# Performance work log

Hardware: AMD Instinct MI355X
Metric: run time of the kernel (lower is better)

## Reference

```python
import jax, jax.numpy as jnp
from jax import lax
import numpy as np

# cfg constants (not present in snippet; fixed realistic values)
GAMMA = 5.0            # cfg.RISK_AVERSION
COST_COEFF = 1e-3      # cfg.COST_COEFF
ALPHA = 0.95           # cfg.CVAR_CONFIDENCE
KAPPA = 2.0627128075074256  # norm.pdf(norm.ppf(0.95)) / (1 - 0.95)
PEN_XI = 100.0
N_ITERS = 500
LR = 0.01

B, H, N = 128, 12, 100


def setup_inputs() -> dict:
    key = jax.random.key(0)
    k1, k2, k3, k4 = jax.random.split(key, 4)
    mu = 0.02 * jax.random.normal(k1, (B, H, N), dtype=jnp.float32)
    # factor scale so that sigma_p = ||L^T w|| is O(0.02) for diversified w
    L = 0.02 * jax.random.normal(k2, (B, H, N, N), dtype=jnp.float32)
    w_prev = jax.random.uniform(k3, (B, N), dtype=jnp.float32)
    w_prev = w_prev / jnp.sum(w_prev, axis=-1, keepdims=True)  # on simplex
    cvar_limit = 0.05 + 0.05 * jax.random.uniform(k4, (B,), dtype=jnp.float32)
    return {"mu": mu, "L": L, "w_prev": w_prev, "cvar_limit": cvar_limit}


def _project_simplex(v):
    # Euclidean projection of each last-axis vector onto {w >= 0, sum w = 1}
    n = v.shape[-1]
    u = jnp.sort(v, axis=-1)[..., ::-1]
    cssv = jnp.cumsum(u, axis=-1) - 1.0
    ar = jnp.arange(1, n + 1, dtype=v.dtype)
    rho = jnp.sum(u * ar > cssv, axis=-1)          # >= 1 always
    theta = jnp.take_along_axis(cssv, (rho - 1)[..., None], axis=-1)
    theta = theta / rho[..., None].astype(v.dtype)
    return jnp.maximum(v - theta, 0.0)


def _neg_objective(w, mu, L, w_prev, cvar_limit):
    # w: (B,H,N). Exact-penalty reformulation: optimal xi_t = relu(-mu_p + kappa*sigma_p - limit)
    Lw = jnp.einsum('bhnm,bhn->bhm', L, w)             # L[t].T @ w[t]
    ret_t = jnp.einsum('bhn,bhn->bh', mu, w)           # mu[t] @ w[t]
    risk = jnp.sum(Lw * Lw, axis=(1, 2))               # sum_t ||L_t^T w_t||^2
    w_lag = jnp.concatenate([w_prev[:, None, :], w[:, :-1]], axis=1)
    diff = w - w_lag
    cost = jnp.sum(jnp.sqrt(diff * diff + 1e-10), axis=(1, 2))  # smoothed L1 turnover
    sigma = jnp.sqrt(jnp.sum(Lw * Lw, axis=-1) + 1e-12)          # (B,H)
    viol = jnp.maximum(-ret_t + KAPPA * sigma - cvar_limit[:, None], 0.0)
    obj = jnp.sum(ret_t, 1) - GAMMA * risk - COST_COEFF * cost - PEN_XI * jnp.sum(viol, 1)
    return -jnp.sum(obj)


def _solve(mu, L, w_prev, cvar_limit):
    b, h, n = mu.shape
    w0 = jnp.broadcast_to(w_prev[:, None, :], (b, h, n))
    grad_fn = jax.grad(_neg_objective)

    def step(w, _):
        g = grad_fn(w, mu, L, w_prev, cvar_limit)
        return _project_simplex(w - LR * g), None

    w, _ = lax.scan(jax.checkpoint(step), w0, None, length=N_ITERS)
    return w


def reference(mu, L, w_prev, cvar_limit):
    # Batched projected-gradient solver for the same convex MPO program the
    # original solves with SCS via CvxpyLayer; returns the optimal plan w (B,H,N).
    return _solve(mu, L, w_prev, cvar_limit)
```

## Files before the change

### kernel.cpp

```cpp
#include <hip/hip_runtime.h>
#include <cstdint>
#include <cstddef>

#define NIT    500
#define GAMMA_ 5.0f
#define CC_    1e-3f
#define KAPPA_ 2.0627128075074256f
#define PEN_   100.0f
#define LR_    0.01f

#define PBUF_BYTES (128*2*2*100*4)
#define FLAG_COUNT 256

#define VMFENCE() asm volatile("s_waitcnt vmcnt(0)" ::: "memory")
__device__ __forceinline__ float sysLoadF(float* p) {
  return __hip_atomic_fetch_add(p, 0.0f, __ATOMIC_RELAXED, __HIP_MEMORY_SCOPE_SYSTEM);
}
__device__ __forceinline__ void sysStoreF(float* p, float v) {
  (void)__hip_atomic_exchange(p, v, __ATOMIC_RELAXED, __HIP_MEMORY_SCOPE_SYSTEM);
}
__device__ __forceinline__ int sysLoadI(int* p) {
  return __hip_atomic_fetch_add(p, 0, __ATOMIC_RELAXED, __HIP_MEMORY_SCOPE_SYSTEM);
}
__device__ __forceinline__ void sysStoreI(int* p, int v) {
  (void)__hip_atomic_exchange(p, v, __ATOMIC_RELAXED, __HIP_MEMORY_SCOPE_SYSTEM);
}

__device__ __forceinline__ float rdlane(float v, int lane) {
  return __int_as_float(__builtin_amdgcn_readlane(__float_as_int(v), lane));
}

__device__ __forceinline__ float wred64(float x) {
  int t;
  t = __builtin_amdgcn_update_dpp(0, __float_as_int(x), 0x111, 0xf, 0xf, true); x += __int_as_float(t);
  t = __builtin_amdgcn_update_dpp(0, __float_as_int(x), 0x112, 0xf, 0xf, true); x += __int_as_float(t);
  t = __builtin_amdgcn_update_dpp(0, __float_as_int(x), 0x114, 0xf, 0xf, true); x += __int_as_float(t);
  t = __builtin_amdgcn_update_dpp(0, __float_as_int(x), 0x118, 0xf, 0xf, true); x += __int_as_float(t);
  t = __builtin_amdgcn_update_dpp(0, __float_as_int(x), 0x142, 0xa, 0xf, true); x += __int_as_float(t);
  t = __builtin_amdgcn_update_dpp(0, __float_as_int(x), 0x143, 0xc, 0xf, true); x += __int_as_float(t);
  return rdlane(x, 63);
}

__global__ __launch_bounds__(768, 1) void mpo_solver(
    const float* __restrict__ mu, const float* __restrict__ L,
    const float* __restrict__ wprev, const float* __restrict__ climit,
    float* __restrict__ out, float* __restrict__ pbuf, int* __restrict__ flags)
{
  const int tid  = threadIdx.x;
  const int lane = tid & 63;
  const int wave = __builtin_amdgcn_readfirstlane(tid >> 6);
  const int j    = wave >> 1;
  const int sec  = wave & 1;
  const int bid  = blockIdx.x;
  const int b    = bid & 127;
  const int half = bid >> 7;
  const int h    = half * 6 + j;
  const int bh   = b * 12 + h;

  __shared__ float wbuf[2][6][100];
  __shared__ float ybuf[6][100];

  const float* Lb = L + (size_t)bh * 10000;

  float S[100];
#pragma unroll
  for (int c = 0; c < 100; ++c) S[c] = 0.f;
  const int r = sec * 50 + lane;
  if (lane < 50) {
#pragma unroll 1
    for (int mc = 0; mc < 25; ++mc) {
      float4 lr = *(const float4*)(Lb + r * 100 + mc * 4);
#pragma unroll
      for (int c = 0; c < 100; ++c) {
        const float* Lc = Lb + c * 100 + mc * 4;
        S[c] = fmaf(lr.x, Lc[0], fmaf(lr.y, Lc[1], fmaf(lr.z, Lc[2], fmaf(lr.w, Lc[3], S[c]))));
      }
    }
  }

  const bool val1 = (lane < 36);
  float mu0 = mu[(size_t)bh * 100 + lane];
  float mu1 = val1 ? mu[(size_t)bh * 100 + 64 + lane] : 0.f;
  float wp0 = wprev[b * 100 + lane];
  float wp1 = val1 ? wprev[b * 100 + 64 + lane] : 0.f;
  float lim = climit[b];

  float w0 = wp0, w1 = wp1;

  if (sec == 0) {
    wbuf[0][j][lane] = wp0;
    if (val1) wbuf[0][j][64 + lane] = wp1;
  }
  __syncthreads();

  const bool hasNext = (h < 11);
  const bool isPubL  = (half == 0) && (j == 5);
  const bool isPubH  = (half == 1) && (j == 0);
  const int  flagPub = isPubL ? (b * 2 + 0) : (b * 2 + 1);
  const int  flagCon = isPubL ? (b * 2 + 1) : (b * 2 + 0);
  const bool isCon   = (sec == 0) && (isPubL || isPubH);
  bool dead = false;
  float thp = -3.0e38f;

  for (int k = 0; k < NIT; ++k) {
    const int p = k & 1;

    float yloc;
    {
      float a0 = 0.f, a1 = 0.f, a2 = 0.f, a3 = 0.f;
      const float* wrow = wbuf[p][j];
#pragma unroll
      for (int q = 0; q < 25; ++q) {
        float4 wq = *(const float4*)(wrow + q * 4);
        a0 = fmaf(wq.x, S[q * 4 + 0], a0);
        a1 = fmaf(wq.y, S[q * 4 + 1], a1);
        a2 = fmaf(wq.z, S[q * 4 + 2], a2);
        a3 = fmaf(wq.w, S[q * 4 + 3], a3);
      }
      yloc = (a0 + a2) + (a1 + a3);
      if (sec == 1 && lane < 50) ybuf[j][50 + lane] = yloc;
    }

    float pf0 = 0.f, pf1 = 0.f;
    bool pfReady = false;
    if (isCon && k > 0) {
      if (sysLoadI(&flags[flagCon]) >= k) {
        float* src = pbuf + ((size_t)flagCon * 2 + (k & 1)) * 100;
        pf0 = sysLoadF(&src[lane]);
        pf1 = val1 ? sysLoadF(&src[64 + lane]) : 0.f;
        pfReady = true;
      }
    }
    __syncthreads();

    if (sec == 0) {
      float y0 = (lane < 50) ? yloc : ybuf[j][lane];
      float y1 = val1 ? ybuf[j][64 + lane] : 0.f;

      float ret = wred64(fmaf(mu0, w0, mu1 * w1));
      float s2  = wred64(fmaf(y0, w0, y1 * w1));
      float sigma = sqrtf(s2 + 1e-12f);
      float z     = KAPPA_ * sigma - ret - lim;
      float act   = (z > 0.f) ? 1.f : 0.f;
      float cY    = 2.f * GAMMA_ + act * (PEN_ * KAPPA_ / sigma);
      float cM    = -(1.f + act * PEN_);

      float wl0, wl1, wn0 = 0.f, wn1 = 0.f;
      if (j == 0) {
        if (half == 0 || k == 0) { wl0 = wp0; wl1 = wp1; }
        else {
          if (!pfReady) {
            if (!dead) {
              long guard = 0;
              while (sysLoadI(&flags[flagCon]) < k) {
                __builtin_amdgcn_s_sleep(2);
                if (++guard > (1L << 17)) { dead = true; break; }
              }
            }
            float* src = pbuf + ((size_t)flagCon * 2 + (k & 1)) * 100;
            pf0 = sysLoadF(&src[lane]);
            pf1 = val1 ? sysLoadF(&src[64 + lane]) : 0.f;
          }
          wl0 = pf0; wl1 = pf1;
        }
      } else { wl0 = wbuf[p][j - 1][lane]; wl1 = val1 ? wbuf[p][j - 1][64 + lane] : 0.f; }
      if (hasNext) {
        if (j == 5) {
          if (k == 0) { wn0 = wp0; wn1 = wp1; }
          else {
            if (!pfReady) {
              if (!dead) {
                long guard = 0;
                while (sysLoadI(&flags[flagCon]) < k) {
                  __builtin_amdgcn_s_sleep(2);
                  if (++guard > (1L << 17)) { dead = true; break; }
                }
              }
              float* src = pbuf + ((size_t)flagCon * 2 + (k & 1)) * 100;
              pf0 = sysLoadF(&src[lane]);
              pf1 = val1 ? sysLoadF(&src[64 + lane]) : 0.f;
            }
            wn0 = pf0; wn1 = pf1;
          }
        } else { wn0 = wbuf[p][j + 1][lane]; wn1 = val1 ? wbuf[p][j + 1][64 + lane] : 0.f; }
      }

      float dw0 = w0 - wl0;
      float g0  = fmaf(cM, mu0, cY * y0) + CC_ * (dw0 * rsqrtf(fmaf(dw0, dw0, 1e-10f)));
      if (hasNext) { float dn0 = wn0 - w0; g0 -= CC_ * (dn0 * rsqrtf(fmaf(dn0, dn0, 1e-10f))); }
      float v0 = fmaf(-LR_, g0, w0);
      float v1 = 0.f;
      if (val1) {
        float dw1 = w1 - wl1;
        float g1  = fmaf(cM, mu1, cY * y1) + CC_ * (dw1 * rsqrtf(fmaf(dw1, dw1, 1e-10f)));
        if (hasNext) { float dn1 = wn1 - w1; g1 -= CC_ * (dn1 * rsqrtf(fmaf(dn1, dn1, 1e-10f))); }
        v1 = fmaf(-LR_, g1, w1);
      }

      float a1m = val1 ? 1.f : 0.f;
      float na0 = (v0 > thp) ? 1.f : 0.f;
      float na1 = (val1 && (v1 > thp)) ? 1.f : 0.f;
      float Ssum = wred64(na0 * v0 + na1 * v1);
      float Cnt  = wred64(na0 + na1);
      if (Cnt < 0.5f) { Ssum = wred64(v0 + a1m * v1); Cnt = 100.f; }
      float theta = (Ssum - 1.f) / Cnt;
      for (int it = 0; it < 112; ++it) {
        na0 = (v0 > theta) ? 1.f : 0.f;
        na1 = (val1 && (v1 > theta)) ? 1.f : 0.f;
        float ns = wred64(na0 * v0 + na1 * v1);
        float nc = wred64(na0 + na1);
        if (nc == Cnt && ns == Ssum) break;
        if (it == 7) {
          ns = wred64(v0 + a1m * v1);
          nc = 100.f;
        }
        Ssum = ns; Cnt = nc;
        theta = (Ssum - 1.f) / Cnt;
      }
      thp = theta;
      w0 = fmaxf(v0 - theta, 0.f);
      w1 = val1 ? fmaxf(v1 - theta, 0.f) : 0.f;

      wbuf[1 - p][j][lane] = w0;
      if (val1) wbuf[1 - p][j][64 + lane] = w1;

      if (isPubL || isPubH) {
        float* dst = pbuf + ((size_t)flagPub * 2 + ((k + 1) & 1)) * 100;
        sysStoreF(&dst[lane], w0);
        if (val1) sysStoreF(&dst[64 + lane], w1);
        if (lane == 0) {
          VMFENCE();
          sysStoreI(&flags[flagPub], k + 1);
        }
      }
    }
    __syncthreads();
  }

  if (sec == 0) {
    float* o = out + (size_t)bh * 100;
    o[lane] = w0;
    if (val1) o[64 + lane] = w1;
  }
}

extern "C" void kernel_launch(void* const* d_in, const int* in_sizes, int n_in,
                              void* d_out, int out_size, void* d_ws, size_t ws_size,
                              hipStream_t stream) {
  const float* mu = (const float*)d_in[0];
  const float* L  = (const float*)d_in[1];
  const float* wp = (const float*)d_in[2];
  const float* cl = (const float*)d_in[3];
  float* pbuf  = (float*)d_ws;
  int*   flags = (int*)((char*)d_ws + PBUF_BYTES);
  hipMemsetAsync(flags, 0, FLAG_COUNT * sizeof(int), stream);
  hipLaunchKernelGGL(mpo_solver, dim3(256), dim3(768), 0, stream,
                     mu, L, wp, cl, (float*)d_out, pbuf, flags);
}
```

Before: 1.897 ms.

## Replace per-iteration block barriers with point-to-point LDS flag synchronization

Removes the two __syncthreads per solver iteration and splits the workgroup into a matvec helper wave and a solver wave per horizon step. The two sides coordinate through per-wave LDS flags (ybuf ready, wbuf ready) using acquire/release atomics and spin-waits. Each wave now waits only on its own helper and its neighbouring horizon waves, not on all 12 waves. This is meant to cut the block-wide stall on every iteration and let waves drift out of lockstep. In exchange it adds spin loops with sleeps and relies on subtle ordering across the double-buffered wbuf.

```diff
diff --git a/kernel.cpp b/kernel.cpp
--- a/kernel.cpp
+++ b/kernel.cpp
@@ -24,6 +24,12 @@
 }
 __device__ __forceinline__ void sysStoreI(int* p, int v) {
   (void)__hip_atomic_exchange(p, v, __ATOMIC_RELAXED, __HIP_MEMORY_SCOPE_SYSTEM);
+}
+__device__ __forceinline__ int ldsLoadAcq(int* p) {
+  return __hip_atomic_load(p, __ATOMIC_ACQUIRE, __HIP_MEMORY_SCOPE_WORKGROUP);
+}
+__device__ __forceinline__ void ldsStoreRel(int* p, int v) {
+  __hip_atomic_store(p, v, __ATOMIC_RELEASE, __HIP_MEMORY_SCOPE_WORKGROUP);
 }
 
 __device__ __forceinline__ float rdlane(float v, int lane) {
@@ -59,6 +65,8 @@
 
   __shared__ float wbuf[2][6][100];
   __shared__ float ybuf[6][100];
+  __shared__ int   yf[6];
+  __shared__ int   wf[6];
 
   const float* Lb = L + (size_t)bh * 10000;
 
@@ -85,12 +93,11 @@
   float wp1 = val1 ? wprev[b * 100 + 64 + lane] : 0.f;
   float lim = climit[b];
 
-  float w0 = wp0, w1 = wp1;
-
   if (sec == 0) {
     wbuf[0][j][lane] = wp0;
     if (val1) wbuf[0][j][64 + lane] = wp1;
   }
+  if (tid < 6) { wf[tid] = 0; yf[tid] = 0; }
   __syncthreads();
 
   const bool hasNext = (h < 11);
@@ -98,17 +105,19 @@
   const bool isPubH  = (half == 1) && (j == 0);
   const int  flagPub = isPubL ? (b * 2 + 0) : (b * 2 + 1);
   const int  flagCon = isPubL ? (b * 2 + 1) : (b * 2 + 0);
-  const bool isCon   = (sec == 0) && (isPubL || isPubH);
   bool dead = false;
-  float thp = -3.0e38f;
-
-  for (int k = 0; k < NIT; ++k) {
-    const int p = k & 1;
-
-    float yloc;
-    {
+
+  if (sec == 1) {
+    for (int k = 0; k < NIT; ++k) {
+      if (!dead && ldsLoadAcq(&wf[j]) < k) {
+        long g = 0;
+        while (ldsLoadAcq(&wf[j]) < k) {
+          __builtin_amdgcn_s_sleep(1);
+          if (++g > (1L << 18)) { dead = true; break; }
+        }
+      }
       float a0 = 0.f, a1 = 0.f, a2 = 0.f, a3 = 0.f;
-      const float* wrow = wbuf[p][j];
+      const float* wrow = wbuf[k & 1][j];
 #pragma unroll
       for (int q = 0; q < 25; ++q) {
         float4 wq = *(const float4*)(wrow + q * 4);
@@ -117,44 +126,51 @@
         a2 = fmaf(wq.z, S[q * 4 + 2], a2);
         a3 = fmaf(wq.w, S[q * 4 + 3], a3);
       }
-      yloc = (a0 + a2) + (a1 + a3);
-      if (sec == 1 && lane < 50) ybuf[j][50 + lane] = yloc;
+      if (lane < 50) ybuf[j][50 + lane] = (a0 + a2) + (a1 + a3);
+      if (lane == 0) ldsStoreRel(&yf[j], k + 1);
     }
-
-    float pf0 = 0.f, pf1 = 0.f;
-    bool pfReady = false;
-    if (isCon && k > 0) {
-      if (sysLoadI(&flags[flagCon]) >= k) {
-        float* src = pbuf + ((size_t)flagCon * 2 + (k & 1)) * 100;
-        pf0 = sysLoadF(&src[lane]);
-        pf1 = val1 ? sysLoadF(&src[64 + lane]) : 0.f;
-        pfReady = true;
-      }
-    }
-    __syncthreads();
-
-    if (sec == 0) {
-      float y0 = (lane < 50) ? yloc : ybuf[j][lane];
-      float y1 = val1 ? ybuf[j][64 + lane] : 0.f;
-
-      float ret = wred64(fmaf(mu0, w0, mu1 * w1));
-      float s2  = wred64(fmaf(y0, w0, y1 * w1));
-      float sigma = sqrtf(s2 + 1e-12f);
-      float z     = KAPPA_ * sigma - ret - lim;
-      float act   = (z > 0.f) ? 1.f : 0.f;
-      float cY    = 2.f * GAMMA_ + act * (PEN_ * KAPPA_ / sigma);
-      float cM    = -(1.f + act * PEN_);
+  } else {
+    float w0 = wp0, w1 = wp1;
+    float thp = -3.0e38f;
+    for (int k = 0; k < NIT; ++k) {
+      const int p = k & 1;
+
+      float yloc;
+      {
+        float a0 = 0.f, a1 = 0.f, a2 = 0.f, a3 = 0.f;
+        const float* wrow = wbuf[p][j];
+#pragma unroll
+        for (int q = 0; q < 25; ++q) {
+          float4 wq = *(const float4*)(wrow + q * 4);
+          a0 = fmaf(wq.x, S[q * 4 + 0], a0);
+          a1 = fmaf(wq.y, S[q * 4 + 1], a1);
+          a2 = fmaf(wq.z, S[q * 4 + 2], a2);
+          a3 = fmaf(wq.w, S[q * 4 + 3], a3);
+        }
+        yloc = (a0 + a2) + (a1 + a3);
+      }
+
+      float pf0 = 0.f, pf1 = 0.f;
+      bool pfReady = false;
+      if ((isPubL || isPubH) && k > 0) {
+        if (sysLoadI(&flags[flagCon]) >= k) {
+          float* src = pbuf + ((size_t)flagCon * 2 + (k & 1)) * 100;
+          pf0 = sysLoadF(&src[lane]);
+          pf1 = val1 ? sysLoadF(&src[64 + lane]) : 0.f;
+          pfReady = true;
+        }
+      }
 
       float wl0, wl1, wn0 = 0.f, wn1 = 0.f;
       if (j == 0) {
         if (half == 0 || k == 0) { wl0 = wp0; wl1 = wp1; }
         else {
           if (!pfReady) {
-            if (!dead) {
-              long guard = 0;
+            if (!dead && sysLoadI(&flags[flagCon]) < k) {
+              long g = 0;
               while (sysLoadI(&flags[flagCon]) < k) {
                 __builtin_amdgcn_s_sleep(2);
-                if (++guard > (1L << 17)) { dead = true; break; }
+                if (++g > (1L << 17)) { dead = true; break; }
               }
             }
             float* src = pbuf + ((size_t)flagCon * 2 + (k & 1)) * 100;
@@ -163,17 +179,27 @@
           }
           wl0 = pf0; wl1 = pf1;
         }
-      } else { wl0 = wbuf[p][j - 1][lane]; wl1 = val1 ? wbuf[p][j - 1][64 + lane] : 0.f; }
+      } else {
+        if (!dead && ldsLoadAcq(&wf[j - 1]) < k) {
+          long g = 0;
+          while (ldsLoadAcq(&wf[j - 1]) < k) {
+            __builtin_amdgcn_s_sleep(1);
+            if (++g > (1L << 18)) { dead = true; break; }
+          }
+        }
+        wl0 = wbuf[p][j - 1][lane];
+        wl1 = val1 ? wbuf[p][j - 1][64 + lane] : 0.f;
+      }
       if (hasNext) {
         if (j == 5) {
           if (k == 0) { wn0 = wp0; wn1 = wp1; }
           else {
             if (!pfReady) {
-              if (!dead) {
-                long guard = 0;
+              if (!dead && sysLoadI(&flags[flagCon]) < k) {
+                long g = 0;
                 while (sysLoadI(&flags[flagCon]) < k) {
                   __builtin_amdgcn_s_sleep(2);
-                  if (++guard > (1L << 17)) { dead = true; break; }
+                  if (++g > (1L << 17)) { dead = true; break; }
                 }
               }
               float* src = pbuf + ((size_t)flagCon * 2 + (k & 1)) * 100;
@@ -182,8 +208,36 @@
             }
             wn0 = pf0; wn1 = pf1;
           }
-        } else { wn0 = wbuf[p][j + 1][lane]; wn1 = val1 ? wbuf[p][j + 1][64 + lane] : 0.f; }
-      }
+        } else {
+          if (!dead && ldsLoadAcq(&wf[j + 1]) < k) {
+            long g = 0;
+            while (ldsLoadAcq(&wf[j + 1]) < k) {
+              __builtin_amdgcn_s_sleep(1);
+              if (++g > (1L << 18)) { dead = true; break; }
+            }
+          }
+          wn0 = wbuf[p][j + 1][lane];
+          wn1 = val1 ? wbuf[p][j + 1][64 + lane] : 0.f;
+        }
+      }
+
+      if (!dead && ldsLoadAcq(&yf[j]) < k + 1) {
+        long g = 0;
+        while (ldsLoadAcq(&yf[j]) < k + 1) {
+          __builtin_amdgcn_s_sleep(1);
+          if (++g > (1L << 18)) { dead = true; break; }
+        }
+      }
+      float y0 = (lane < 50) ? yloc : ybuf[j][lane];
+      float y1 = val1 ? ybuf[j][64 + lane] : 0.f;
+
+      float ret = wred64(fmaf(mu0, w0, mu1 * w1));
+      float s2  = wred64(fmaf(y0, w0, y1 * w1));
+      float sigma = sqrtf(s2 + 1e-12f);
+      float z     = KAPPA_ * sigma - ret - lim;
+      float act   = (z > 0.f) ? 1.f : 0.f;
+      float cY    = 2.f * GAMMA_ + act * (PEN_ * KAPPA_ / sigma);
+      float cM    = -(1.f + act * PEN_);
 
       float dw0 = w0 - wl0;
       float g0  = fmaf(cM, mu0, cY * y0) + CC_ * (dw0 * rsqrtf(fmaf(dw0, dw0, 1e-10f)));
@@ -223,6 +277,7 @@
 
       wbuf[1 - p][j][lane] = w0;
       if (val1) wbuf[1 - p][j][64 + lane] = w1;
+      if (lane == 0) ldsStoreRel(&wf[j], k + 1);
 
       if (isPubL || isPubH) {
         float* dst = pbuf + ((size_t)flagPub * 2 + ((k + 1) & 1)) * 100;
@@ -234,10 +289,7 @@
         }
       }
     }
-    __syncthreads();
-  }
-
-  if (sec == 0) {
+
     float* o = out + (size_t)bh * 100;
     o[lane] = w0;
     if (val1) o[64 + lane] = w1;
```

Result: slower. 4.224 ms (+122.6%).
